# Performance work log

Hardware: AMD Instinct MI355X
Metric: run time of the kernel (lower is better)

## Reference

```python
import jax, jax.numpy as jnp
import numpy as np

B, S, F_IN, D, H, DFF, L = 64, 256, 64, 512, 8, 2048, 6
A_DIM, FEAT, OUT = 8, 32, 5
EPS = 1e-3  # keras default epsilon for BatchNorm/LayerNorm


def _sinusoidal_pes(seq_len, d_model):
    pos = np.arange(seq_len)[:, None].astype(np.float32)
    i = np.arange(d_model)[None, :].astype(np.float32)
    angle = pos / np.power(10000.0, (2.0 * np.floor(i / 2.0)) / d_model)
    pe = np.zeros((seq_len, d_model), dtype=np.float32)
    pe[:, 0::2] = np.sin(angle[:, 0::2])
    pe[:, 1::2] = np.cos(angle[:, 1::2])
    return jnp.asarray(pe)


def setup_inputs() -> dict:
    key = jax.random.key(0)
    ks = jax.random.split(key, 16)
    w = lambda k, shape: 0.02 * jax.random.normal(k, shape, dtype=jnp.float32)
    return {
        'state': jax.random.normal(ks[0], (B, S, F_IN), dtype=jnp.float32),
        'action': jax.random.normal(ks[1], (B, A_DIM), dtype=jnp.float32),
        'pes': _sinusoidal_pes(S, D),
        'W_emb': w(ks[2], (F_IN, D)), 'b_emb': jnp.zeros((D,), jnp.float32),
        'Wq': w(ks[3], (L, D, D)), 'bq': jnp.zeros((L, D), jnp.float32),
        'Wk': w(ks[4], (L, D, D)), 'bk': jnp.zeros((L, D), jnp.float32),
        'Wv': w(ks[5], (L, D, D)), 'bv': jnp.zeros((L, D), jnp.float32),
        'Wo': w(ks[6], (L, D, D)), 'bo': jnp.zeros((L, D), jnp.float32),
        'bn_gamma': jnp.ones((L, D), jnp.float32), 'bn_beta': jnp.zeros((L, D), jnp.float32),
        'W1': w(ks[7], (L, D, DFF)), 'b1': jnp.zeros((L, DFF), jnp.float32),
        'W2': w(ks[8], (L, DFF, D)), 'b2': jnp.zeros((L, D), jnp.float32),
        'ln_gamma': jnp.ones((L, D), jnp.float32), 'ln_beta': jnp.zeros((L, D), jnp.float32),
        'Wf': w(ks[9], (S * D, FEAT)), 'bf': jnp.zeros((FEAT,), jnp.float32),
        'Wfin': w(ks[10], (FEAT + A_DIM, OUT)), 'bfin': jnp.zeros((OUT,), jnp.float32),
    }


def _encoder(x, pes, layer_params):
    # x: [B, S, D]
    x = x + pes  # positional encoding

    def step(h, p):
        Wq, bq, Wk, bk, Wv, bv, Wo, bo, gb, bb, W1, b1, W2, b2, gl, bl = p
        b, s, d = h.shape
        dh = d // H
        q = (h @ Wq + bq).reshape(b, s, H, dh)
        k = (h @ Wk + bk).reshape(b, s, H, dh)
        v = (h @ Wv + bv).reshape(b, s, H, dh)
        scores = jnp.einsum('bqhd,bkhd->bhqk', q, k) / jnp.sqrt(jnp.asarray(dh, h.dtype))
        attn = jax.nn.softmax(scores, axis=-1)
        ctx = jnp.einsum('bhqk,bkhd->bqhd', attn, v).reshape(b, s, d)
        ctx = ctx @ Wo + bo
        y = h + ctx
        # BatchNormalization over (batch, seq), per-channel (training-mode batch stats)
        mu = y.mean(axis=(0, 1))
        var = y.var(axis=(0, 1))
        y = gb * (y - mu) * jax.lax.rsqrt(var + EPS) + bb
        # FFN + residual + LayerNorm
        f = jax.nn.relu(y @ W1 + b1) @ W2 + b2
        z = y + f
        mu2 = z.mean(axis=-1, keepdims=True)
        var2 = z.var(axis=-1, keepdims=True)
        z = gl * (z - mu2) * jax.lax.rsqrt(var2 + EPS) + bl
        return z, None

    x, _ = jax.lax.scan(step, x, layer_params)
    return x


def reference(state, action, pes, W_emb, b_emb, Wq, bq, Wk, bk, Wv, bv, Wo, bo,
              bn_gamma, bn_beta, W1, b1, W2, b2, ln_gamma, ln_beta, Wf, bf, Wfin, bfin):
    x = state @ W_emb + b_emb                       # [B, S, D]
    layer_params = (Wq, bq, Wk, bk, Wv, bv, Wo, bo, bn_gamma, bn_beta,
                    W1, b1, W2, b2, ln_gamma, ln_beta)
    enc = _encoder(x, pes, layer_params)            # [B, S, D]
    flat = enc.reshape(enc.shape[0], -1)            # [B, S*D]
    feat = flat @ Wf + bf                           # [B, 32]
    out = jnp.concatenate([feat, action], axis=-1) @ Wfin + bfin  # [B, 5]
    return out
```

## Files before the change

### kernel.cpp

```cpp
#include <hip/hip_runtime.h>

typedef short bf16x8 __attribute__((ext_vector_type(8)));
typedef float f32x4 __attribute__((ext_vector_type(4)));
typedef unsigned short us;

#define BN_EPS 1e-3f

static __device__ __forceinline__ us f2bs(float x) {
  unsigned int u = __builtin_bit_cast(unsigned int, x);
  unsigned int r = (u + 0x7FFFu + ((u >> 16) & 1u)) >> 16;
  return (us)r;
}
static __device__ __forceinline__ float b2f(us v) {
  unsigned int u = (unsigned int)v << 16;
  return __builtin_bit_cast(float, u);
}

static __device__ __forceinline__ void gl_lds16(const us* g, us* l) {
  __builtin_amdgcn_global_load_lds(
      (const __attribute__((address_space(1))) void*)g,
      (__attribute__((address_space(3))) void*)l, 16, 0, 0);
}

__global__ __launch_bounds__(256) void transpose_bf16(
    const float* __restrict__ src, us* __restrict__ dst, int K, int N,
    long sstride, long dstride) {
  long sbs = (long)blockIdx.z * sstride;
  long sbd = (long)blockIdx.z * dstride;
  __shared__ float tile[32][33];
  int tx = threadIdx.x & 31, ty = threadIdx.x >> 5;
  int k0 = blockIdx.x * 32, n0 = blockIdx.y * 32;
  for (int i = 0; i < 32; i += 8)
    tile[ty + i][tx] = src[sbs + (long)(k0 + ty + i) * N + n0 + tx];
  __syncthreads();
  for (int i = 0; i < 32; i += 8)
    dst[sbd + (long)(n0 + ty + i) * K + k0 + tx] = f2bs(tile[tx][ty + i]);
}

__global__ __launch_bounds__(256) void embed_kernel(
    const float* __restrict__ state, const float* __restrict__ Wemb,
    const float* __restrict__ bemb, const float* __restrict__ pes,
    us* __restrict__ hb) {
  int t = threadIdx.x;
  int row0 = blockIdx.x * 8;
  __shared__ float st[8][64];
  {
    int i = t;
    st[i >> 6][i & 63] = state[(long)row0 * 64 + i];
    i += 256;
    st[i >> 6][i & 63] = state[(long)row0 * 64 + i];
  }
  __syncthreads();
  int c0 = t, c1 = t + 256;
  float acc0[8], acc1[8];
#pragma unroll
  for (int r = 0; r < 8; ++r) { acc0[r] = 0.f; acc1[r] = 0.f; }
  for (int kk = 0; kk < 64; ++kk) {
    float w0 = Wemb[kk * 512 + c0], w1 = Wemb[kk * 512 + c1];
#pragma unroll
    for (int r = 0; r < 8; ++r) {
      acc0[r] += st[r][kk] * w0;
      acc1[r] += st[r][kk] * w1;
    }
  }
  float be0 = bemb[c0], be1 = bemb[c1];
#pragma unroll
  for (int r = 0; r < 8; ++r) {
    int row = row0 + r, s = row & 255;
    hb[(long)row * 512 + c0] = f2bs(acc0[r] + be0 + pes[(long)s * 512 + c0]);
    hb[(long)row * 512 + c1] = f2bs(acc1[r] + be1 + pes[(long)s * 512 + c1]);
  }
}

enum { EPI_QKV = 0, EPI_RESID_BF16 = 1, EPI_RELU_BF16 = 2, EPI_FFN2_BF16 = 3,
       EPI_FEAT = 4 };

template <int BM, int BN, int WM, int WN, int EPI>
__global__ __launch_bounds__((BM / WM) * (BN / WN) * 64)
void gemm_bt(const us* __restrict__ A, int lda, long batchA,
             const us* __restrict__ Bt, int ldb, long batchB,
             void* __restrict__ Cout, void* __restrict__ C2,
             void* __restrict__ C3, int ldc,
             const float* __restrict__ bias,
             const us* __restrict__ resid,
             const float* __restrict__ gsum, const float* __restrict__ gsumsq,
             const float* __restrict__ gamma, const float* __restrict__ beta,
             int K) {
  constexpr int WCols = BN / WN;
  constexpr int NT = (BM / WM) * (BN / WN) * 64;
  constexpr int NW = NT / 64;
  constexpr int MI = WM / 16, NI = WN / 16;
  constexpr int LA = BM / 8;
  constexpr int LB = BN / 8;
  const int tid = threadIdx.x;
  const int w = tid >> 6, l = tid & 63;
  const int wr = w / WCols, wc = w % WCols;
  const int lr = l & 15, lh = l >> 4;
  const int z = blockIdx.z;
  const long m0 = (long)blockIdx.x * BM;
  const long n0 = (long)blockIdx.y * BN;
  A += (long)z * batchA;
  Bt += (long)z * batchB;
  __shared__ __align__(16) us smem[BM * 64 + BN * 64];
  us* Asm = smem;
  us* Bsm = smem + BM * 64;
  const int srow = l >> 3, scol = (l & 7) << 3;
  f32x4 acc[MI][NI] = {};
  for (int kt = 0; kt < K; kt += 64) {
    __syncthreads();
    for (int j = w; j < LA; j += NW) {
      int rb = j * 8;
      gl_lds16(A + (m0 + rb + srow) * lda + kt + scol, Asm + rb * 64);
    }
    for (int j = w; j < LB; j += NW) {
      int rb = j * 8;
      gl_lds16(Bt + (n0 + rb + srow) * ldb + kt + scol, Bsm + rb * 64);
    }
    asm volatile("s_waitcnt vmcnt(0)" ::: "memory");
    __syncthreads();
#pragma unroll
    for (int kk = 0; kk < 64; kk += 32) {
      bf16x8 af[MI], bfr[NI];
#pragma unroll
      for (int mi = 0; mi < MI; ++mi)
        af[mi] = *(const bf16x8*)&Asm[(wr * WM + mi * 16 + lr) * 64 + kk + lh * 8];
#pragma unroll
      for (int ni = 0; ni < NI; ++ni)
        bfr[ni] = *(const bf16x8*)&Bsm[(wc * WN + ni * 16 + lr) * 64 + kk + lh * 8];
#pragma unroll
      for (int mi = 0; mi < MI; ++mi)
#pragma unroll
        for (int ni = 0; ni < NI; ++ni)
          acc[mi][ni] = __builtin_amdgcn_mfma_f32_16x16x32_bf16(
              af[mi], bfr[ni], acc[mi][ni], 0, 0, 0);
    }
  }

  if constexpr (EPI == EPI_QKV) {
    const int seg = (int)(n0 >> 9);
    const int nc0 = (int)(n0 & 511);
    if (seg == 2) {
#pragma unroll
      for (int mi = 0; mi < MI; ++mi) {
#pragma unroll
        for (int ni = 0; ni < NI; ++ni) {
          const int segc = nc0 + wc * WN + ni * 16 + lr;
          const float bv_ = beta[segc];
          ushort4 pv;
#pragma unroll
          for (int q_ = 0; q_ < 4; ++q_)
            ((us*)&pv)[q_] = f2bs(acc[mi][ni][q_] + bv_);
          const long row0g = m0 + wr * WM + mi * 16 + lh * 4;
          const long o = (((row0g >> 8) * 8 + (segc >> 6)) * 64 + (segc & 63)) *
                             256 + (row0g & 255);
          *(ushort4*)&((us*)C3)[o] = pv;
        }
      }
    } else {
      __syncthreads();
#pragma unroll
      for (int mi = 0; mi < MI; ++mi)
#pragma unroll
        for (int ni = 0; ni < NI; ++ni) {
          const int cl = wc * WN + ni * 16 + lr;
          const float bv_ = seg == 0 ? bias[nc0 + cl] : gamma[nc0 + cl];
#pragma unroll
          for (int q_ = 0; q_ < 4; ++q_) {
            const int rl = wr * WM + mi * 16 + lh * 4 + q_;
            smem[rl * BN + cl] = f2bs(acc[mi][ni][q_] + bv_);
          }
        }
      __syncthreads();
      us* dstp = seg == 0 ? (us*)Cout : (us*)C2;
      for (int i = tid; i < (BM * BN) / 8; i += NT) {
        const int idx = i * 8;
        const int row = idx / BN, colc = idx % BN;
        *(uint4*)&dstp[(m0 + row) * 512 + nc0 + colc] = *(uint4*)&smem[idx];
      }
    }
  } else if constexpr ((EPI == EPI_RELU_BF16 || EPI == EPI_RESID_BF16 ||
                        EPI == EPI_FFN2_BF16) && BM == 128 && BN == 128) {
    __syncthreads();
#pragma unroll
    for (int mi = 0; mi < MI; ++mi)
#pragma unroll
      for (int ni = 0; ni < NI; ++ni) {
        const int cl = wc * WN + ni * 16 + lr;
        const int col = (int)n0 + cl;
        const float bv_ = bias[col];
        float aa = 0.f, bb2 = 0.f;
        if constexpr (EPI == EPI_FFN2_BF16) {
          aa = gsum[col];
          bb2 = gsumsq[col];
        }
#pragma unroll
        for (int q_ = 0; q_ < 4; ++q_) {
          const int rl = wr * WM + mi * 16 + lh * 4 + q_;
          float v = acc[mi][ni][q_] + bv_;
          if constexpr (EPI == EPI_RELU_BF16) {
            smem[rl * BN + cl] = f2bs(fmaxf(v, 0.f));
          } else if constexpr (EPI == EPI_RESID_BF16) {
            v += b2f(resid[(m0 + rl) * ldc + col]);
            smem[rl * BN + cl] = f2bs(v);
          } else {
            float ybn = b2f(resid[(m0 + rl) * ldc + col]) * aa + bb2;
            smem[rl * BN + cl] = f2bs(ybn + v);
          }
        }
      }
    __syncthreads();
    for (int i = tid; i < (BM * BN) / 8; i += NT) {
      const int idx = i * 8;
      const int row = idx / BN, colc = idx % BN;
      *(uint4*)&((us*)Cout)[(m0 + row) * ldc + n0 + colc] = *(uint4*)&smem[idx];
    }
  } else {
#pragma unroll
    for (int mi = 0; mi < MI; ++mi) {
#pragma unroll
      for (int ni = 0; ni < NI; ++ni) {
        const int col = (int)n0 + wc * WN + ni * 16 + lr;
#pragma unroll
        for (int q_ = 0; q_ < 4; ++q_) {
          const long row = m0 + wr * WM + mi * 16 + lh * 4 + q_;
          if constexpr (EPI == EPI_FEAT) {
            atomicAdd(&((float*)Cout)[row * ldc + col], acc[mi][ni][q_]);
          }
        }
      }
    }
  }
}

__global__ __launch_bounds__(256) void attn_kernel(
    const us* __restrict__ q, const us* __restrict__ k,
    const us* __restrict__ vt, us* __restrict__ ctx) {
  const int half = blockIdx.x;
  const int z = blockIdx.y;
  const int b = z >> 3, hh = z & 7;
  const long qkBase = (long)b * 131072 + hh * 64;
  const int tid = threadIdx.x, w = tid >> 6, l = tid & 63;
  const int lr = l & 15, lh = l >> 4;
  __shared__ __align__(16) us Qs[32][72];
  __shared__ __align__(16) us Ks[64][72];
  __shared__ __align__(16) us Pb[32][264];
  __shared__ float fred[32][2];
  const int qr = (w >> 1) * 16, qc = (w & 1) * 32;
  const us* vb = vt + (long)z * 16384;
  const int ldr = tid >> 3, ldc = (tid & 7) << 3;

  for (int qi = 0; qi < 4; ++qi) {
    const int qb = half * 4 + qi;
    *(uint4*)&Qs[ldr][ldc] =
        *(const uint4*)(q + qkBase + (long)(qb * 32 + ldr) * 512 + ldc);
    f32x4 sacc[4][2] = {};
    for (int skb = 0; skb < 4; ++skb) {
      __syncthreads();
      for (int i = tid; i < 512; i += 256) {
        int r = i >> 3, c = (i & 7) << 3;
        *(uint4*)&Ks[r][c] =
            *(const uint4*)(k + qkBase + (long)(skb * 64 + r) * 512 + c);
      }
      __syncthreads();
#pragma unroll
      for (int kh = 0; kh < 2; ++kh) {
        bf16x8 aq = *(const bf16x8*)&Qs[qr + lr][kh * 32 + lh * 8];
#pragma unroll
        for (int ni = 0; ni < 2; ++ni) {
          bf16x8 bkk = *(const bf16x8*)&Ks[qc + ni * 16 + lr][kh * 32 + lh * 8];
          sacc[skb][ni] = __builtin_amdgcn_mfma_f32_16x16x32_bf16(
              aq, bkk, sacc[skb][ni], 0, 0, 0);
        }
      }
    }
    float m0[4] = {-1e30f, -1e30f, -1e30f, -1e30f};
#pragma unroll
    for (int skb = 0; skb < 4; ++skb)
#pragma unroll
      for (int ni = 0; ni < 2; ++ni)
#pragma unroll
        for (int q_ = 0; q_ < 4; ++q_) {
          float v = sacc[skb][ni][q_] * 0.125f;
          sacc[skb][ni][q_] = v;
          m0[q_] = fmaxf(m0[q_], v);
        }
#pragma unroll
    for (int off = 1; off < 16; off <<= 1)
#pragma unroll
      for (int q_ = 0; q_ < 4; ++q_)
        m0[q_] = fmaxf(m0[q_], __shfl_xor(m0[q_], off));
    if (lr == 0) {
#pragma unroll
      for (int q_ = 0; q_ < 4; ++q_) fred[qr + lh * 4 + q_][w & 1] = m0[q_];
    }
    __syncthreads();
#pragma unroll
    for (int q_ = 0; q_ < 4; ++q_) {
      int row = qr + lh * 4 + q_;
      m0[q_] = fmaxf(fred[row][0], fred[row][1]);
    }
    float s0[4] = {0.f, 0.f, 0.f, 0.f};
#pragma unroll
    for (int skb = 0; skb < 4; ++skb)
#pragma unroll
      for (int ni = 0; ni < 2; ++ni)
#pragma unroll
        for (int q_ = 0; q_ < 4; ++q_) {
          float e = __expf(sacc[skb][ni][q_] - m0[q_]);
          sacc[skb][ni][q_] = e;
          s0[q_] += e;
        }
#pragma unroll
    for (int off = 1; off < 16; off <<= 1)
#pragma unroll
      for (int q_ = 0; q_ < 4; ++q_) s0[q_] += __shfl_xor(s0[q_], off);
    __syncthreads();
    if (lr == 0) {
#pragma unroll
      for (int q_ = 0; q_ < 4; ++q_) fred[qr + lh * 4 + q_][w & 1] = s0[q_];
    }
    __syncthreads();
#pragma unroll
    for (int q_ = 0; q_ < 4; ++q_) {
      int row = qr + lh * 4 + q_;
      s0[q_] = 1.f / (fred[row][0] + fred[row][1]);
    }
#pragma unroll
    for (int skb = 0; skb < 4; ++skb)
#pragma unroll
      for (int ni = 0; ni < 2; ++ni)
#pragma unroll
        for (int q_ = 0; q_ < 4; ++q_)
          Pb[qr + lh * 4 + q_][skb * 64 + qc + ni * 16 + lr] =
              f2bs(sacc[skb][ni][q_] * s0[q_]);
    f32x4 pacc[2] = {};
    for (int kc = 0; kc < 256; kc += 64) {
      __syncthreads();
      for (int i = tid; i < 512; i += 256) {
        int r = i >> 3, c = (i & 7) << 3;
        *(uint4*)&Ks[r][c] = *(const uint4*)(vb + (long)r * 256 + kc + c);
      }
      __syncthreads();
#pragma unroll
      for (int kh = 0; kh < 2; ++kh) {
        bf16x8 ap = *(const bf16x8*)&Pb[qr + lr][kc + kh * 32 + lh * 8];
#pragma unroll
        for (int ni = 0; ni < 2; ++ni) {
          bf16x8 bv2 = *(const bf16x8*)&Ks[qc + ni * 16 + lr][kh * 32 + lh * 8];
          pacc[ni] = __builtin_amdgcn_mfma_f32_16x16x32_bf16(
              ap, bv2, pacc[ni], 0, 0, 0);
        }
      }
    }
    const long cb2 = ((long)(b * 256 + qb * 32)) * 512 + hh * 64;
#pragma unroll
    for (int ni = 0; ni < 2; ++ni)
#pragma unroll
      for (int q_ = 0; q_ < 4; ++q_) {
        int row = qr + lh * 4 + q_;
        int col = qc + ni * 16 + lr;
        ctx[cb2 + (long)row * 512 + col] = f2bs(pacc[ni][q_]);
      }
  }
}

__global__ __launch_bounds__(256) void bn_stats(const us* __restrict__ y,
                                                float* __restrict__ gsum,
                                                float* __restrict__ gsumsq) {
  int t = threadIdx.x;
  long base = (long)blockIdx.x * 64 * 512;
  float s0 = 0, q0 = 0, s1 = 0, q1 = 0;
  for (int r = 0; r < 64; ++r) {
    ushort2 v = *(const ushort2*)(y + base + r * 512 + 2 * t);
    float v0 = b2f(v.x), v1 = b2f(v.y);
    s0 += v0; q0 += v0 * v0;
    s1 += v1; q1 += v1 * v1;
  }
  atomicAdd(&gsum[2 * t], s0);
  atomicAdd(&gsumsq[2 * t], q0);
  atomicAdd(&gsum[2 * t + 1], s1);
  atomicAdd(&gsumsq[2 * t + 1], q1);
}

__global__ void bn_coef(float* __restrict__ gsum, float* __restrict__ gsumsq,
                        const float* __restrict__ gamma,
                        const float* __restrict__ beta) {
  int c = blockIdx.x * 256 + threadIdx.x;
  if (c < 512) {
    const float invN = 1.f / 16384.f;
    float mu = gsum[c] * invN;
    float var = gsumsq[c] * invN - mu * mu;
    float a = gamma[c] * rsqrtf(var + BN_EPS);
    float b = beta[c] - mu * a;
    gsum[c] = a;
    gsumsq[c] = b;
  }
}

__global__ __launch_bounds__(256) void fold_w1(
    const us* __restrict__ W1T, const float* __restrict__ aa,
    const float* __restrict__ bb, const float* __restrict__ b1,
    us* __restrict__ W1s, float* __restrict__ bias1f) {
  int n = blockIdx.x * 4 + (threadIdx.x >> 6);
  int l = threadIdx.x & 63;
  int k0 = l * 8;
  const us* row = W1T + (long)n * 512;
  us tmp[8], outv[8];
  *(uint4*)tmp = *(const uint4*)(row + k0);
  float dot = 0.f;
#pragma unroll
  for (int j = 0; j < 8; ++j) {
    float wv = b2f(tmp[j]);
    dot += bb[k0 + j] * wv;
    outv[j] = f2bs(aa[k0 + j] * wv);
  }
  *(uint4*)(W1s + (long)n * 512 + k0) = *(uint4*)outv;
  for (int off = 32; off >= 1; off >>= 1) dot += __shfl_down(dot, off);
  if (l == 0) bias1f[n] = b1[n] + dot;
}

__global__ __launch_bounds__(128) void ln_kernel(
    const us* __restrict__ zin, const float* __restrict__ g,
    const float* __restrict__ b, us* __restrict__ hb) {
  int r = blockIdx.x, t = threadIdx.x;
  const us* zr = zin + (long)r * 512;
  ushort4 vz = *(const ushort4*)(zr + t * 4);
  float v0 = b2f(((us*)&vz)[0]), v1 = b2f(((us*)&vz)[1]);
  float v2 = b2f(((us*)&vz)[2]), v3 = b2f(((us*)&vz)[3]);
  float s = v0 + v1 + v2 + v3;
  float qs = v0 * v0 + v1 * v1 + v2 * v2 + v3 * v3;
  for (int off = 32; off >= 1; off >>= 1) {
    s += __shfl_down(s, off);
    qs += __shfl_down(qs, off);
  }
  __shared__ float ls[2], lq[2];
  if ((t & 63) == 0) {
    ls[t >> 6] = s;
    lq[t >> 6] = qs;
  }
  __syncthreads();
  float mu = (ls[0] + ls[1]) * (1.f / 512.f);
  float var = (lq[0] + lq[1]) * (1.f / 512.f) - mu * mu;
  float rs = rsqrtf(var + BN_EPS);
  float4 gg = *(const float4*)(g + t * 4);
  float4 bb = *(const float4*)(b + t * 4);
  ushort4 hv;
  ((us*)&hv)[0] = f2bs(gg.x * (v0 - mu) * rs + bb.x);
  ((us*)&hv)[1] = f2bs(gg.y * (v1 - mu) * rs + bb.y);
  ((us*)&hv)[2] = f2bs(gg.z * (v2 - mu) * rs + bb.z);
  ((us*)&hv)[3] = f2bs(gg.w * (v3 - mu) * rs + bb.w);
  *(ushort4*)(hb + (long)r * 512 + t * 4) = hv;
}

__global__ void zerof(float* __restrict__ p, int n) {
  int i = blockIdx.x * 256 + threadIdx.x;
  if (i < n) p[i] = 0.f;
}

__global__ __launch_bounds__(320) void final_head(
    const float* __restrict__ feat, const float* __restrict__ bf_,
    const float* __restrict__ action, const float* __restrict__ Wfin,
    const float* __restrict__ bfin, float* __restrict__ out) {
  int t = threadIdx.x;
  int b = t & 63, o = t >> 6;
  float acc = bfin[o];
  for (int j = 0; j < 32; ++j) acc += (feat[b * 32 + j] + bf_[j]) * Wfin[j * 5 + o];
  for (int j = 0; j < 8; ++j) acc += action[b * 8 + j] * Wfin[(32 + j) * 5 + o];
  out[b * 5 + o] = acc;
}

extern "C" void kernel_launch(void* const* d_in, const int* in_sizes, int n_in,
                              void* d_out, int out_size, void* d_ws,
                              size_t ws_size, hipStream_t stream) {
  const float* state = (const float*)d_in[0];
  const float* action = (const float*)d_in[1];
  const float* pes = (const float*)d_in[2];
  const float* W_emb = (const float*)d_in[3];
  const float* b_emb = (const float*)d_in[4];
  const float* Wq = (const float*)d_in[5];
  const float* bq = (const float*)d_in[6];
  const float* Wk = (const float*)d_in[7];
  const float* bk = (const float*)d_in[8];
  const float* Wv = (const float*)d_in[9];
  const float* bv = (const float*)d_in[10];
  const float* Wo = (const float*)d_in[11];
  const float* bo = (const float*)d_in[12];
  const float* bn_g = (const float*)d_in[13];
  const float* bn_b = (const float*)d_in[14];
  const float* W1 = (const float*)d_in[15];
  const float* b1 = (const float*)d_in[16];
  const float* W2 = (const float*)d_in[17];
  const float* b2 = (const float*)d_in[18];
  const float* ln_g = (const float*)d_in[19];
  const float* ln_b = (const float*)d_in[20];
  const float* Wf = (const float*)d_in[21];
  const float* bf_ = (const float*)d_in[22];
  const float* Wfin = (const float*)d_in[23];
  const float* bfin = (const float*)d_in[24];
  float* out = (float*)d_out;
  (void)in_sizes; (void)n_in; (void)out_size;

  char* wp = (char*)d_ws;
  size_t off = 0;
  auto take = [&](size_t bytes) {
    void* p = wp + off;
    off += (bytes + 255) & ~(size_t)255;
    return p;
  };
  us* qkvT = (us*)take(6ull * 1536 * 512 * 2);
  us* WoT = (us*)take(6ull * 512 * 512 * 2);
  us* W1T = (us*)take(6ull * 2048 * 512 * 2);
  us* W2T = (us*)take(6ull * 512 * 2048 * 2);
  us* WfT = (us*)take(32ull * 131072 * 2);
  us* hb = (us*)take(16384ull * 512 * 2);
  us* ybf = (us*)take(16384ull * 512 * 2);
  us* W1s = (us*)take(2048ull * 512 * 2);
  float* bias1f = (float*)take(2048 * 4);
  us* qb_ = (us*)take(16384ull * 512 * 2);
  us* kb_ = (us*)take(16384ull * 512 * 2);
  us* vt = (us*)take(16384ull * 512 * 2);
  us* bigR4 = (us*)take(33554432ull * 2);
  float* gsum = (float*)take(512 * 4);
  float* gsumsq = (float*)take(512 * 4);
  float* feat = (float*)take(2048 * 4);
  us* ctxb = bigR4;
  us* f1 = bigR4;
  us* zbf = qb_;

  if (off > ws_size) return;

  transpose_bf16<<<dim3(16, 16, 6), 256, 0, stream>>>(Wq, qkvT, 512, 512,
                                                      262144, 786432);
  transpose_bf16<<<dim3(16, 16, 6), 256, 0, stream>>>(Wk, qkvT + 262144, 512,
                                                      512, 262144, 786432);
  transpose_bf16<<<dim3(16, 16, 6), 256, 0, stream>>>(Wv, qkvT + 524288, 512,
                                                      512, 262144, 786432);
  transpose_bf16<<<dim3(16, 16, 6), 256, 0, stream>>>(Wo, WoT, 512, 512,
                                                      262144, 262144);
  transpose_bf16<<<dim3(16, 64, 6), 256, 0, stream>>>(W1, W1T, 512, 2048,
                                                      1048576, 1048576);
  transpose_bf16<<<dim3(64, 16, 6), 256, 0, stream>>>(W2, W2T, 2048, 512,
                                                      1048576, 1048576);
  transpose_bf16<<<dim3(4096, 1, 1), 256, 0, stream>>>(Wf, WfT, 131072, 32,
                                                       0, 0);
  embed_kernel<<<2048, 256, 0, stream>>>(state, W_emb, b_emb, pes, hb);

  for (int l = 0; l < 6; ++l) {
    const us* qkvTl = qkvT + (size_t)l * 786432;
    const us* WoTl = WoT + (size_t)l * 262144;
    const us* W1Tl = W1T + (size_t)l * 1048576;
    const us* W2Tl = W2T + (size_t)l * 1048576;

    gemm_bt<128, 128, 64, 64, EPI_QKV><<<dim3(128, 12, 1), 256, 0, stream>>>(
        hb, 512, 0, qkvTl, 512, 0, qb_, kb_, vt, 512, bq + l * 512,
        nullptr, nullptr, nullptr, bk + l * 512, bv + l * 512, 512);
    attn_kernel<<<dim3(2, 512), 256, 0, stream>>>(qb_, kb_, vt, ctxb);
    gemm_bt<128, 128, 64, 64, EPI_RESID_BF16><<<dim3(128, 4, 1), 256, 0, stream>>>(
        ctxb, 512, 0, WoTl, 512, 0, ybf, nullptr, nullptr, 512, bo + l * 512,
        hb, nullptr, nullptr, nullptr, nullptr, 512);
    zerof<<<4, 256, 0, stream>>>(gsum, 1024);
    bn_stats<<<256, 256, 0, stream>>>(ybf, gsum, gsumsq);
    bn_coef<<<2, 256, 0, stream>>>(gsum, gsumsq, bn_g + l * 512,
                                   bn_b + l * 512);
    fold_w1<<<512, 256, 0, stream>>>(W1Tl, gsum, gsumsq, b1 + l * 2048, W1s,
                                     bias1f);
    gemm_bt<128, 128, 64, 64, EPI_RELU_BF16><<<dim3(128, 16, 1), 256, 0, stream>>>(
        ybf, 512, 0, W1s, 512, 0, f1, nullptr, nullptr, 2048, bias1f,
        nullptr, nullptr, nullptr, nullptr, nullptr, 512);
    gemm_bt<128, 128, 64, 64, EPI_FFN2_BF16><<<dim3(128, 4, 1), 256, 0, stream>>>(
        f1, 2048, 0, W2Tl, 2048, 0, zbf, nullptr, nullptr, 512, b2 + l * 512,
        ybf, gsum, gsumsq, nullptr, nullptr, 2048);
    ln_kernel<<<16384, 128, 0, stream>>>(zbf, ln_g + l * 512, ln_b + l * 512,
                                         hb);
  }

  zerof<<<8, 256, 0, stream>>>(feat, 2048);
  gemm_bt<64, 32, 32, 16, EPI_FEAT><<<dim3(1, 1, 128), 256, 0, stream>>>(
      hb, 131072, 1024, WfT, 131072, 1024, feat, nullptr, nullptr, 32,
      nullptr, nullptr, nullptr, nullptr, nullptr, nullptr, 1024);
  final_head<<<1, 320, 0, stream>>>(feat, bf_, action, Wfin, bfin, out);
}
```

Measured before the change: 1.596 ms.

## Add 256x256 tiled GEMM with 4-stage LDS pipeline for QKV and FFN1

Introduces a new 512-thread GEMM kernel with 256x256 output tiles and K-step 32. It uses a 4-slot global_load_lds ring buffer with swizzled LDS layout, split A/B prefetch interleaved with MFMA phases, and s_setprio around the MFMA blocks. QKV and FFN1 projections switch to it, cutting the block count and raising data reuse per tile. The trade-offs are 128KB of LDS per block, which limits occupancy, and fewer blocks (384/512) to spread across the CUs, which risks tail imbalance.

```diff
diff --git a/kernel.cpp b/kernel.cpp
--- a/kernel.cpp
+++ b/kernel.cpp
@@ -74,6 +74,155 @@
 
 enum { EPI_QKV = 0, EPI_RESID_BF16 = 1, EPI_RELU_BF16 = 2, EPI_FFN2_BF16 = 3,
        EPI_FEAT = 4 };
+
+template <int EPI>
+__global__ __launch_bounds__(512, 2) void gemm256(
+    const us* __restrict__ A, int lda, const us* __restrict__ Bt, int ldb,
+    void* __restrict__ Cout, void* __restrict__ C2, void* __restrict__ C3,
+    int ldc, const float* __restrict__ bias, const us* __restrict__ resid,
+    const float* __restrict__ gamma, const float* __restrict__ beta, int K) {
+  const int tid = threadIdx.x;
+  const int w = tid >> 6, l = tid & 63;
+  const int wr = w >> 2, wc = w & 3;
+  const int lr = l & 15, lh = l >> 4;
+  const long m0 = (long)blockIdx.x * 256;
+  const long n0 = (long)blockIdx.y * 256;
+  const int KC = K >> 5;
+  __shared__ __align__(16) us sh[4 * 16384];
+  const int o = tid * 16;
+  const int lg = o ^ ((o >> 2) & 0x30);
+  const int sr = lg >> 6;
+  const int sc = (lg & 63) >> 1;
+  const int pb = lr * 32 + ((lh * 8) ^ ((lr & 3) << 3));
+  const us* Asl = sh + wr * 4096 + pb;
+  const us* Bsl = sh + 8192 + (wc >> 1) * 4096 + (wc & 1) * 2048 + pb;
+
+  for (int j = 0; j < 3; ++j) {
+    us* slot = sh + j * 16384;
+    gl_lds16(A + (m0 + sr) * lda + j * 32 + sc, slot + tid * 8);
+    gl_lds16(A + (m0 + 128 + sr) * lda + j * 32 + sc, slot + 4096 + tid * 8);
+    gl_lds16(Bt + (n0 + sr) * ldb + j * 32 + sc, slot + 8192 + tid * 8);
+    gl_lds16(Bt + (n0 + 128 + sr) * ldb + j * 32 + sc, slot + 12288 + tid * 8);
+  }
+  asm volatile("s_waitcnt vmcnt(8)" ::: "memory");
+  __builtin_amdgcn_s_barrier();
+
+  f32x4 acc[8][4] = {};
+  for (int c = 0; c < KC; ++c) {
+    const int soff = (c & 3) * 16384;
+    const bool st = (c + 3) < KC;
+    us* nslot = sh + ((c + 3) & 3) * 16384;
+    const int nk = (c + 3) * 32;
+    if (st) {
+      gl_lds16(A + (m0 + sr) * lda + nk + sc, nslot + tid * 8);
+      gl_lds16(A + (m0 + 128 + sr) * lda + nk + sc, nslot + 4096 + tid * 8);
+    }
+    bf16x8 bfr[4], af[4];
+#pragma unroll
+    for (int ni = 0; ni < 4; ++ni)
+      bfr[ni] = *(const bf16x8*)(Bsl + soff + ni * 512);
+#pragma unroll
+    for (int mi = 0; mi < 4; ++mi)
+      af[mi] = *(const bf16x8*)(Asl + soff + mi * 512);
+    __builtin_amdgcn_s_barrier();
+    __builtin_amdgcn_s_setprio(1);
+#pragma unroll
+    for (int mi = 0; mi < 4; ++mi)
+#pragma unroll
+      for (int ni = 0; ni < 4; ++ni)
+        acc[mi][ni] = __builtin_amdgcn_mfma_f32_16x16x32_bf16(
+            af[mi], bfr[ni], acc[mi][ni], 0, 0, 0);
+    __builtin_amdgcn_s_setprio(0);
+    __builtin_amdgcn_s_barrier();
+    if (st) {
+      gl_lds16(Bt + (n0 + sr) * ldb + nk + sc, nslot + 8192 + tid * 8);
+      gl_lds16(Bt + (n0 + 128 + sr) * ldb + nk + sc, nslot + 12288 + tid * 8);
+    }
+#pragma unroll
+    for (int mi = 0; mi < 4; ++mi)
+      af[mi] = *(const bf16x8*)(Asl + soff + (mi + 4) * 512);
+    __builtin_amdgcn_s_barrier();
+    __builtin_amdgcn_s_setprio(1);
+#pragma unroll
+    for (int mi = 0; mi < 4; ++mi)
+#pragma unroll
+      for (int ni = 0; ni < 4; ++ni)
+        acc[mi + 4][ni] = __builtin_amdgcn_mfma_f32_16x16x32_bf16(
+            af[mi], bfr[ni], acc[mi + 4][ni], 0, 0, 0);
+    __builtin_amdgcn_s_setprio(0);
+    if (c < KC - 3)
+      asm volatile("s_waitcnt vmcnt(8)" ::: "memory");
+    else if (c == KC - 3)
+      asm volatile("s_waitcnt vmcnt(4)" ::: "memory");
+    else if (c == KC - 2)
+      asm volatile("s_waitcnt vmcnt(0)" ::: "memory");
+    __builtin_amdgcn_s_barrier();
+  }
+  if constexpr (EPI == EPI_QKV) {
+    const int seg = (int)(n0 >> 9);
+    const int nc0 = (int)(n0 & 511);
+    if (seg == 2) {
+#pragma unroll
+      for (int mi = 0; mi < 8; ++mi)
+#pragma unroll
+        for (int ni = 0; ni < 4; ++ni) {
+          const int segc = nc0 + wc * 64 + ni * 16 + lr;
+          const float bv_ = beta[segc];
+          ushort4 pv;
+#pragma unroll
+          for (int q_ = 0; q_ < 4; ++q_)
+            ((us*)&pv)[q_] = f2bs(acc[mi][ni][q_] + bv_);
+          const long row0g = m0 + wr * 128 + mi * 16 + lh * 4;
+          const long oo =
+              (((row0g >> 8) * 8 + (segc >> 6)) * 64 + (segc & 63)) * 256 +
+              (row0g & 255);
+          *(ushort4*)&((us*)C3)[oo] = pv;
+        }
+    } else {
+#pragma unroll
+      for (int mi = 0; mi < 8; ++mi)
+#pragma unroll
+        for (int ni = 0; ni < 4; ++ni) {
+          const int cl = wc * 64 + ni * 16 + lr;
+          const float bv_ = seg == 0 ? bias[nc0 + cl] : gamma[nc0 + cl];
+#pragma unroll
+          for (int q_ = 0; q_ < 4; ++q_) {
+            const int rl = wr * 128 + mi * 16 + lh * 4 + q_;
+            sh[rl * 256 + cl] = f2bs(acc[mi][ni][q_] + bv_);
+          }
+        }
+      asm volatile("s_waitcnt lgkmcnt(0)" ::: "memory");
+      __builtin_amdgcn_s_barrier();
+      us* dstp = seg == 0 ? (us*)Cout : (us*)C2;
+      for (int i = tid; i < 8192; i += 512) {
+        const int idx = i * 8;
+        const int row = idx >> 8, col = idx & 255;
+        *(uint4*)&dstp[(m0 + row) * 512 + nc0 + col] = *(uint4*)&sh[idx];
+      }
+    }
+  } else {
+#pragma unroll
+    for (int mi = 0; mi < 8; ++mi)
+#pragma unroll
+      for (int ni = 0; ni < 4; ++ni) {
+        const int cl = wc * 64 + ni * 16 + lr;
+        const float bv_ = bias[(int)n0 + cl];
+#pragma unroll
+        for (int q_ = 0; q_ < 4; ++q_) {
+          const int rl = wr * 128 + mi * 16 + lh * 4 + q_;
+          sh[rl * 256 + cl] = f2bs(fmaxf(acc[mi][ni][q_] + bv_, 0.f));
+        }
+      }
+    asm volatile("s_waitcnt lgkmcnt(0)" ::: "memory");
+    __builtin_amdgcn_s_barrier();
+    for (int i = tid; i < 8192; i += 512) {
+      const int idx = i * 8;
+      const int row = idx >> 8, col = idx & 255;
+      *(uint4*)&((us*)Cout)[(m0 + row) * ldc + n0 + col] = *(uint4*)&sh[idx];
+    }
+  }
+  (void)resid;
+}
 
 template <int BM, int BN, int WM, int WN, int EPI>
 __global__ __launch_bounds__((BM / WM) * (BN / WN) * 64)
@@ -136,50 +285,8 @@
     }
   }
 
-  if constexpr (EPI == EPI_QKV) {
-    const int seg = (int)(n0 >> 9);
-    const int nc0 = (int)(n0 & 511);
-    if (seg == 2) {
-#pragma unroll
-      for (int mi = 0; mi < MI; ++mi) {
-#pragma unroll
-        for (int ni = 0; ni < NI; ++ni) {
-          const int segc = nc0 + wc * WN + ni * 16 + lr;
-          const float bv_ = beta[segc];
-          ushort4 pv;
-#pragma unroll
-          for (int q_ = 0; q_ < 4; ++q_)
-            ((us*)&pv)[q_] = f2bs(acc[mi][ni][q_] + bv_);
-          const long row0g = m0 + wr * WM + mi * 16 + lh * 4;
-          const long o = (((row0g >> 8) * 8 + (segc >> 6)) * 64 + (segc & 63)) *
-                             256 + (row0g & 255);
-          *(ushort4*)&((us*)C3)[o] = pv;
-        }
-      }
-    } else {
-      __syncthreads();
-#pragma unroll
-      for (int mi = 0; mi < MI; ++mi)
-#pragma unroll
-        for (int ni = 0; ni < NI; ++ni) {
-          const int cl = wc * WN + ni * 16 + lr;
-          const float bv_ = seg == 0 ? bias[nc0 + cl] : gamma[nc0 + cl];
-#pragma unroll
-          for (int q_ = 0; q_ < 4; ++q_) {
-            const int rl = wr * WM + mi * 16 + lh * 4 + q_;
-            smem[rl * BN + cl] = f2bs(acc[mi][ni][q_] + bv_);
-          }
-        }
-      __syncthreads();
-      us* dstp = seg == 0 ? (us*)Cout : (us*)C2;
-      for (int i = tid; i < (BM * BN) / 8; i += NT) {
-        const int idx = i * 8;
-        const int row = idx / BN, colc = idx % BN;
-        *(uint4*)&dstp[(m0 + row) * 512 + nc0 + colc] = *(uint4*)&smem[idx];
-      }
-    }
-  } else if constexpr ((EPI == EPI_RELU_BF16 || EPI == EPI_RESID_BF16 ||
-                        EPI == EPI_FFN2_BF16) && BM == 128 && BN == 128) {
+  if constexpr ((EPI == EPI_RESID_BF16 || EPI == EPI_FFN2_BF16) &&
+                BM == 128 && BN == 128) {
     __syncthreads();
 #pragma unroll
     for (int mi = 0; mi < MI; ++mi)
@@ -197,9 +304,7 @@
         for (int q_ = 0; q_ < 4; ++q_) {
           const int rl = wr * WM + mi * 16 + lh * 4 + q_;
           float v = acc[mi][ni][q_] + bv_;
-          if constexpr (EPI == EPI_RELU_BF16) {
-            smem[rl * BN + cl] = f2bs(fmaxf(v, 0.f));
-          } else if constexpr (EPI == EPI_RESID_BF16) {
+          if constexpr (EPI == EPI_RESID_BF16) {
             v += b2f(resid[(m0 + rl) * ldc + col]);
             smem[rl * BN + cl] = f2bs(v);
           } else {
@@ -230,6 +335,7 @@
       }
     }
   }
+  (void)C2; (void)C3; (void)gamma; (void)beta;
 }
 
 __global__ __launch_bounds__(256) void attn_kernel(
@@ -551,9 +657,9 @@
     const us* W1Tl = W1T + (size_t)l * 1048576;
     const us* W2Tl = W2T + (size_t)l * 1048576;
 
-    gemm_bt<128, 128, 64, 64, EPI_QKV><<<dim3(128, 12, 1), 256, 0, stream>>>(
-        hb, 512, 0, qkvTl, 512, 0, qb_, kb_, vt, 512, bq + l * 512,
-        nullptr, nullptr, nullptr, bk + l * 512, bv + l * 512, 512);
+    gemm256<EPI_QKV><<<dim3(64, 6), 512, 0, stream>>>(
+        hb, 512, qkvTl, 512, qb_, kb_, vt, 512, bq + l * 512, nullptr,
+        bk + l * 512, bv + l * 512, 512);
     attn_kernel<<<dim3(2, 512), 256, 0, stream>>>(qb_, kb_, vt, ctxb);
     gemm_bt<128, 128, 64, 64, EPI_RESID_BF16><<<dim3(128, 4, 1), 256, 0, stream>>>(
         ctxb, 512, 0, WoTl, 512, 0, ybf, nullptr, nullptr, 512, bo + l * 512,
@@ -564,9 +670,9 @@
                                    bn_b + l * 512);
     fold_w1<<<512, 256, 0, stream>>>(W1Tl, gsum, gsumsq, b1 + l * 2048, W1s,
                                      bias1f);
-    gemm_bt<128, 128, 64, 64, EPI_RELU_BF16><<<dim3(128, 16, 1), 256, 0, stream>>>(
-        ybf, 512, 0, W1s, 512, 0, f1, nullptr, nullptr, 2048, bias1f,
-        nullptr, nullptr, nullptr, nullptr, nullptr, 512);
+    gemm256<EPI_RELU_BF16><<<dim3(64, 8), 512, 0, stream>>>(
+        ybf, 512, W1s, 512, f1, nullptr, nullptr, 2048, bias1f, nullptr,
+        nullptr, nullptr, 512);
     gemm_bt<128, 128, 64, 64, EPI_FFN2_BF16><<<dim3(128, 4, 1), 256, 0, stream>>>(
         f1, 2048, 0, W2Tl, 2048, 0, zbf, nullptr, nullptr, 512, b2 + l * 512,
         ybf, gsum, gsumsq, nullptr, nullptr, 2048);
```

New measurement: 1.617 ms. About the same (+1.3%).
